# Kernel tuning notes

Measured on AMD Instinct MI355X. Metric: run time of the kernel, lower is better.

## Reference

```python
import jax, jax.numpy as jnp
import numpy as np

N_NODES = 50000
N_EDGES = 400000
LATENT = 128
HIDDEN = 512
N_HEADS = 2          # latent // 64, NodeAttn default num_heads
HEAD_DIM = LATENT // N_HEADS
N_GRAPHS = 500
LN_EPS = 1e-5


def setup_inputs() -> dict:
    key = jax.random.key(0)
    ks = jax.random.split(key, 24)
    s = 0.02
    inp = {
        "edges": jax.random.randint(ks[0], (2, N_EDGES), 0, N_NODES, dtype=jnp.int32),
        "node_feat": jax.random.normal(ks[1], (N_NODES, LATENT), jnp.float32),
        "edge_attr": jax.random.normal(ks[2], (N_EDGES, LATENT), jnp.float32),
        "u": jax.random.normal(ks[3], (N_GRAPHS, LATENT), jnp.float32),
        "num_nodes": jnp.full((N_GRAPHS,), N_NODES // N_GRAPHS, jnp.int32),
        # NodeAttn params (shared for sent/received calls, as in the module)
        "w1": jax.random.normal(ks[4], (3 * LATENT, LATENT), jnp.float32) * s,
        "b1": jnp.zeros((LATENT,), jnp.float32),
        "w2": jax.random.normal(ks[5], (N_HEADS, HEAD_DIM), jnp.float32) * s,
        "w3": jax.random.normal(ks[6], (2 * LATENT, LATENT), jnp.float32) * s,
        "b3": jnp.zeros((LATENT,), jnp.float32),
        # Encoder MLP: 4*latent -> hidden -> hidden -> latent, LN before ReLU
        "mw0": jax.random.normal(ks[7], (4 * LATENT, HIDDEN), jnp.float32) * s,
        "mb0": jnp.zeros((HIDDEN,), jnp.float32),
        "ls0": jnp.ones((HIDDEN,), jnp.float32),
        "lb0": jnp.zeros((HIDDEN,), jnp.float32),
        "mw1": jax.random.normal(ks[8], (HIDDEN, HIDDEN), jnp.float32) * s,
        "mb1": jnp.zeros((HIDDEN,), jnp.float32),
        "ls1": jnp.ones((HIDDEN,), jnp.float32),
        "lb1": jnp.zeros((HIDDEN,), jnp.float32),
        "mw2": jax.random.normal(ks[9], (HIDDEN, LATENT), jnp.float32) * s,
        "mb2": jnp.zeros((LATENT,), jnp.float32),
    }
    return inp


def _layer_norm(x, scale, bias):
    mu = jnp.mean(x, axis=-1, keepdims=True)
    var = jnp.mean(jnp.square(x - mu), axis=-1, keepdims=True)
    return (x - mu) * jax.lax.rsqrt(var + LN_EPS) * scale + bias


def _node_attn(q, k, ea, index, n_nodes, w1, b1, w2, w3, b3):
    # per-edge multi-head scores -> segment softmax over destination index -> scatter-add
    h = jax.nn.leaky_relu(jnp.concatenate([q, k, ea], axis=-1) @ w1 + b1, 0.2)
    h = h.reshape(-1, N_HEADS, HEAD_DIM)                    # [E, H, D]
    logits = jnp.einsum("ehd,hd->eh", h, w2)                 # [E, H]
    m = jax.ops.segment_max(logits, index, num_segments=n_nodes)
    m = jnp.where(jnp.isfinite(m), m, 0.0)                   # empty segments
    e = jnp.exp(logits - m[index])
    z = jax.ops.segment_sum(e, index, num_segments=n_nodes)
    alpha = e / (z[index] + 1e-16)                           # [E, H]
    v = (jnp.concatenate([k, ea], axis=-1) @ w3 + b3).reshape(-1, N_HEADS, HEAD_DIM)
    out = jax.ops.segment_sum(alpha[..., None] * v, index, num_segments=n_nodes)
    return out.reshape(n_nodes, LATENT)


def reference(edges, node_feat, edge_attr, u, num_nodes, w1, b1, w2, w3, b3,
              mw0, mb0, ls0, lb0, mw1, mb1, ls1, lb1, mw2, mb2):
    n = node_feat.shape[0]
    row, col = edges[0], edges[1]
    sent = _node_attn(node_feat[row], node_feat[col], edge_attr, row, n, w1, b1, w2, w3, b3)
    recv = _node_attn(node_feat[col], node_feat[row], edge_attr, col, n, w1, b1, w2, w3, b3)
    glob = jnp.repeat(u, num_nodes, axis=0, total_repeat_length=n)
    x = jnp.concatenate([node_feat, sent, recv, glob], axis=1)   # [N, 4*latent]
    h = jax.nn.relu(_layer_norm(x @ mw0 + mb0, ls0, lb0))
    h = jax.nn.relu(_layer_norm(h @ mw1 + mb1, ls1, lb1))
    return h @ mw2 + mb2
```

## Files before the change

### kernel.cpp

```cpp
#include <hip/hip_runtime.h>
#include <math.h>

#define LATENT 128

typedef __attribute__((ext_vector_type(8))) short bf16x8;
typedef __attribute__((ext_vector_type(4))) float f32x4;

union U4B { uint4 u; bf16x8 v; };

__device__ __forceinline__ unsigned short f2bf(float f) {
    unsigned int x = __float_as_uint(f);
    unsigned int r = (x + 0x7fffu + ((x >> 16) & 1u)) >> 16;
    return (unsigned short)r;
}
__device__ __forceinline__ float bf2f(unsigned short h) {
    return __uint_as_float(((unsigned int)h) << 16);
}

__global__ void k_gid(const int* __restrict__ num_nodes, int G, int n, int* __restrict__ gid) {
    __shared__ int goff[1025];
    if (threadIdx.x == 0) {
        int acc = 0;
        for (int g = 0; g < G; ++g) { goff[g] = acc; acc += num_nodes[g]; }
        goff[G] = acc;
    }
    __syncthreads();
    for (int g = 0; g < G; ++g) {
        int s = goff[g];
        int e = goff[g + 1]; if (e > n) e = n;
        for (int i = s + (int)threadIdx.x; i < e; i += blockDim.x) gid[i] = g;
    }
}

#define FN  1152
#define FE3 1248
#define FEV 1280
__global__ __launch_bounds__(256) void k_pack2(const float* __restrict__ mw0,
                                               const float* __restrict__ mw1,
                                               const float* __restrict__ mw2,
                                               const float* __restrict__ w1,
                                               const float* __restrict__ w3,
                                               uint4* __restrict__ pw) {
    int tid = blockIdx.x * 256 + threadIdx.x;
    if (tid >= 1312 * 64) return;
    int fid = tid >> 6, lane = tid & 63;
    const float* src; int kt, nt, N;
    if (fid < 512)       { src = mw0;            kt = fid >> 5;           nt = fid & 31;           N = 512; }
    else if (fid < 1024) { src = mw1;            kt = (fid - 512) >> 5;   nt = (fid - 512) & 31;   N = 512; }
    else if (fid < 1152) { src = mw2;            kt = (fid - 1024) >> 3;  nt = (fid - 1024) & 7;   N = 128; }
    else if (fid < 1184) { src = w1;             kt = (fid - 1152) >> 3;  nt = (fid - 1152) & 7;   N = 128; }
    else if (fid < 1216) { src = w1 + 128 * 128; kt = (fid - 1184) >> 3;  nt = (fid - 1184) & 7;   N = 128; }
    else if (fid < 1248) { src = w3;             kt = (fid - 1216) >> 3;  nt = (fid - 1216) & 7;   N = 128; }
    else if (fid < 1280) { src = w1 + 256 * 128; kt = (fid - 1248) >> 3;  nt = (fid - 1248) & 7;   N = 128; }
    else                 { src = w3 + 128 * 128; kt = (fid - 1280) >> 3;  nt = (fid - 1280) & 7;   N = 128; }
    int col = nt * 16 + (lane & 15);
    int k0 = kt * 32 + (lane >> 4) * 8;
    unsigned int w[4];
#pragma unroll
    for (int p = 0; p < 4; ++p) {
        unsigned int lo = f2bf(src[(size_t)(k0 + 2 * p) * N + col]);
        unsigned int hi = f2bf(src[(size_t)(k0 + 2 * p + 1) * N + col]);
        w[p] = lo | (hi << 16);
    }
    pw[(size_t)fid * 64 + lane] = make_uint4(w[0], w[1], w[2], w[3]);
}

__global__ void k_count(const int* __restrict__ edges, int E,
                        int* __restrict__ deg_s, int* __restrict__ deg_r) {
    int e = blockIdx.x * 256 + threadIdx.x;
    if (e < E) { atomicAdd(&deg_s[edges[e]], 1); atomicAdd(&deg_r[edges[E + e]], 1); }
}

__global__ __launch_bounds__(1024) void k_scan(const int* __restrict__ deg, int n,
                                               int* __restrict__ rowptr, int* __restrict__ cursor) {
    __shared__ int part[1025];
    int t = threadIdx.x;
    int chunk = (n + 1023) / 1024;
    int s = t * chunk, epos = s + chunk; if (epos > n) epos = n; if (s > n) s = n;
    int sum = 0;
    for (int i = s; i < epos; ++i) sum += deg[i];
    part[t] = sum;
    __syncthreads();
    if (t == 0) {
        int run = 0;
        for (int i = 0; i < 1024; ++i) { int v = part[i]; part[i] = run; run += v; }
        part[1024] = run;
    }
    __syncthreads();
    int run = part[t];
    for (int i = s; i < epos; ++i) { rowptr[i] = run; cursor[i] = run; run += deg[i]; }
    if (t == 0) rowptr[n] = part[1024];
}

__global__ void k_fill(const int* __restrict__ edges, int E,
                       int* __restrict__ cur_s, int* __restrict__ cur_r,
                       int2* __restrict__ eo_s, int2* __restrict__ eo_r) {
    int e = blockIdx.x * 256 + threadIdx.x;
    if (e < E) {
        int r = edges[e], c = edges[E + e];
        int p = atomicAdd(&cur_s[r], 1); eo_s[p] = make_int2(e, c);
        int q = atomicAdd(&cur_r[c], 1); eo_r[q] = make_int2(e, r);
    }
}

__global__ __launch_bounds__(512) void k_nodepre2(const float* __restrict__ nf, int n,
                                                  const uint4* __restrict__ pw,
                                                  unsigned short* __restrict__ PQK,
                                                  unsigned short* __restrict__ PVh) {
    __shared__ uint4 xs[32 * 64];
    int t = threadIdx.x, lane = t & 63, w = t >> 6;
    int wr = w >> 2, wc = w & 3, l15 = lane & 15, lg = lane >> 4;
    int base = blockIdx.x * 128;
#pragma unroll
    for (int it = 0; it < 4; ++it) {
        int chunk = t + it * 512;
        int row = chunk >> 4, k8 = chunk & 15, k = k8 * 8;
        int node = base + row;
        float4 v0 = make_float4(0.f, 0.f, 0.f, 0.f), v1 = v0;
        if (node < n) {
            const float4* s4 = (const float4*)(nf + (size_t)node * 128 + k);
            v0 = s4[0]; v1 = s4[1];
        }
        uint4 pk;
        pk.x = (unsigned)f2bf(v0.x) | ((unsigned)f2bf(v0.y) << 16);
        pk.y = (unsigned)f2bf(v0.z) | ((unsigned)f2bf(v0.w) << 16);
        pk.z = (unsigned)f2bf(v1.x) | ((unsigned)f2bf(v1.y) << 16);
        pk.w = (unsigned)f2bf(v1.z) | ((unsigned)f2bf(v1.w) << 16);
        int kt = k >> 5, g = (k >> 3) & 3;
        xs[(kt * 8 + (row >> 4)) * 64 + g * 16 + (row & 15)] = pk;
    }
    __syncthreads();
    f32x4 acc[4][6];
#pragma unroll
    for (int rt = 0; rt < 4; ++rt)
#pragma unroll
        for (int ct = 0; ct < 6; ++ct) acc[rt][ct] = (f32x4)(0.f);
    for (int kt = 0; kt < 4; ++kt) {
        U4B a[4];
#pragma unroll
        for (int rt = 0; rt < 4; ++rt) a[rt].u = xs[(kt * 8 + wr * 4 + rt) * 64 + lane];
        U4B b[6];
#pragma unroll
        for (int ct = 0; ct < 6; ++ct) {
            int nt = wc * 6 + ct;
            int mat = nt >> 3, ntm = nt & 7;
            b[ct].u = pw[(size_t)(FN + mat * 32 + kt * 8 + ntm) * 64 + lane];
        }
#pragma unroll
        for (int rt = 0; rt < 4; ++rt)
#pragma unroll
            for (int ct = 0; ct < 6; ++ct)
                acc[rt][ct] = __builtin_amdgcn_mfma_f32_16x16x32_bf16(a[rt].v, b[ct].v, acc[rt][ct], 0, 0, 0);
    }
#pragma unroll
    for (int rt = 0; rt < 4; ++rt)
#pragma unroll
        for (int ct = 0; ct < 6; ++ct) {
            int nt = wc * 6 + ct;
#pragma unroll
            for (int reg = 0; reg < 4; ++reg) {
                int node = base + (wr * 4 + rt) * 16 + lg * 4 + reg;
                if (node < n) {
                    unsigned short hv = f2bf(acc[rt][ct][reg]);
                    if (nt < 16) PQK[(size_t)node * 256 + nt * 16 + l15] = hv;
                    else         PVh[(size_t)node * 128 + (nt - 16) * 16 + l15] = hv;
                }
            }
        }
}

__global__ __launch_bounds__(256) void k_eproj1(const int* __restrict__ edges,
                                                const float* __restrict__ ea, int E,
                                                const uint4* __restrict__ pw,
                                                const unsigned short* __restrict__ PQK,
                                                const float* __restrict__ b1,
                                                const float* __restrict__ w2,
                                                unsigned short* __restrict__ EVg,
                                                float* __restrict__ es, float* __restrict__ er) {
    __shared__ uint4 xs[16 * 64];
    __shared__ unsigned short edata[64 * 128];
    int t = threadIdx.x, lane = t & 63, w = t >> 6;
    int wc = w, l15 = lane & 15, lg = lane >> 4;
    int base = blockIdx.x * 64;
#pragma unroll
    for (int it = 0; it < 4; ++it) {
        int chunk = t + it * 256;
        int row = chunk >> 4, k8 = chunk & 15, k = k8 * 8;
        int e = base + row;
        float4 v0 = make_float4(0.f, 0.f, 0.f, 0.f), v1 = v0;
        if (e < E) {
            const float4* s4 = (const float4*)(ea + (size_t)e * 128 + k);
            v0 = s4[0]; v1 = s4[1];
        }
        uint4 pk;
        pk.x = (unsigned)f2bf(v0.x) | ((unsigned)f2bf(v0.y) << 16);
        pk.y = (unsigned)f2bf(v0.z) | ((unsigned)f2bf(v0.w) << 16);
        pk.z = (unsigned)f2bf(v1.x) | ((unsigned)f2bf(v1.y) << 16);
        pk.w = (unsigned)f2bf(v1.z) | ((unsigned)f2bf(v1.w) << 16);
        int kt = k >> 5, g = (k >> 3) & 3;
        xs[(kt * 4 + (row >> 4)) * 64 + g * 16 + (row & 15)] = pk;
    }
    __syncthreads();
    f32x4 acc[4][4];
#pragma unroll
    for (int rt = 0; rt < 4; ++rt)
#pragma unroll
        for (int ct = 0; ct < 4; ++ct) acc[rt][ct] = (f32x4)(0.f);
    for (int kt = 0; kt < 4; ++kt) {
        U4B a[4];
#pragma unroll
        for (int rt = 0; rt < 4; ++rt) a[rt].u = xs[(kt * 4 + rt) * 64 + lane];
        U4B b[4];
        b[0].u = pw[(size_t)(FE3 + kt * 8 + wc * 2 + 0) * 64 + lane];
        b[1].u = pw[(size_t)(FE3 + kt * 8 + wc * 2 + 1) * 64 + lane];
        b[2].u = pw[(size_t)(FEV + kt * 8 + wc * 2 + 0) * 64 + lane];
        b[3].u = pw[(size_t)(FEV + kt * 8 + wc * 2 + 1) * 64 + lane];
#pragma unroll
        for (int rt = 0; rt < 4; ++rt)
#pragma unroll
            for (int ct = 0; ct < 4; ++ct)
                acc[rt][ct] = __builtin_amdgcn_mfma_f32_16x16x32_bf16(a[rt].v, b[ct].v, acc[rt][ct], 0, 0, 0);
    }
#pragma unroll
    for (int rt = 0; rt < 4; ++rt)
#pragma unroll
        for (int cc = 0; cc < 2; ++cc) {
            int col = (wc * 2 + cc) * 16 + l15;
#pragma unroll
            for (int reg = 0; reg < 4; ++reg) {
                int e_loc = rt * 16 + lg * 4 + reg;
                int e = base + e_loc;
                if (e < E) EVg[(size_t)e * 128 + col] = f2bf(acc[rt][2 + cc][reg]);
                edata[e_loc * 128 + col] = f2bf(acc[rt][cc][reg]);
            }
        }
    __syncthreads();
    int esub = lane >> 3, dg = lane & 7;
    float b1r[16], w2r[16];
    {
        const float4* b4 = (const float4*)(b1 + dg * 16);
        const float4* w4 = (const float4*)(w2 + (dg >> 2) * 64 + (dg & 3) * 16);
#pragma unroll
        for (int q = 0; q < 4; ++q) {
            float4 bv = b4[q], wv = w4[q];
            b1r[q * 4 + 0] = bv.x; b1r[q * 4 + 1] = bv.y; b1r[q * 4 + 2] = bv.z; b1r[q * 4 + 3] = bv.w;
            w2r[q * 4 + 0] = wv.x; w2r[q * 4 + 1] = wv.y; w2r[q * 4 + 2] = wv.z; w2r[q * 4 + 3] = wv.w;
        }
    }
#pragma unroll
    for (int it = 0; it < 2; ++it) {
        int e_loc = w * 16 + it * 8 + esub;
        int e = base + e_loc;
        if (e >= E) break;
        int r = edges[e], c = edges[E + e];
        const uint4* Aqr = (const uint4*)(PQK + ((size_t)r << 8) + dg * 16);
        const uint4* Akc = (const uint4*)(PQK + ((size_t)c << 8) + 128 + dg * 16);
        const uint4* Aqc = (const uint4*)(PQK + ((size_t)c << 8) + dg * 16);
        const uint4* Akr = (const uint4*)(PQK + ((size_t)r << 8) + 128 + dg * 16);
        const uint4* Ae3 = (const uint4*)(&edata[e_loc * 128 + dg * 16]);
        float ps = 0.f, pr = 0.f;
#pragma unroll
        for (int half = 0; half < 2; ++half) {
            uint4 uqr = Aqr[half], ukc = Akc[half], uqc = Aqc[half], ukr = Akr[half], ue3 = Ae3[half];
            unsigned wqr[4] = {uqr.x, uqr.y, uqr.z, uqr.w};
            unsigned wkc[4] = {ukc.x, ukc.y, ukc.z, ukc.w};
            unsigned wqc[4] = {uqc.x, uqc.y, uqc.z, uqc.w};
            unsigned wkr[4] = {ukr.x, ukr.y, ukr.z, ukr.w};
            unsigned we3[4] = {ue3.x, ue3.y, ue3.z, ue3.w};
#pragma unroll
            for (int q = 0; q < 4; ++q) {
#pragma unroll
                for (int hl = 0; hl < 2; ++hl) {
                    int i = half * 8 + q * 2 + hl;
                    float fqr = hl ? __uint_as_float(wqr[q] & 0xffff0000u) : __uint_as_float(wqr[q] << 16);
                    float fkc = hl ? __uint_as_float(wkc[q] & 0xffff0000u) : __uint_as_float(wkc[q] << 16);
                    float fqc = hl ? __uint_as_float(wqc[q] & 0xffff0000u) : __uint_as_float(wqc[q] << 16);
                    float fkr = hl ? __uint_as_float(wkr[q] & 0xffff0000u) : __uint_as_float(wkr[q] << 16);
                    float fe3 = hl ? __uint_as_float(we3[q] & 0xffff0000u) : __uint_as_float(we3[q] << 16);
                    float com = fe3 + b1r[i];
                    float hs = fqr + fkc + com; hs = hs > 0.f ? hs : 0.2f * hs;
                    float hr = fqc + fkr + com; hr = hr > 0.f ? hr : 0.2f * hr;
                    ps += hs * w2r[i]; pr += hr * w2r[i];
                }
            }
        }
        ps += __shfl_xor(ps, 1); ps += __shfl_xor(ps, 2);
        pr += __shfl_xor(pr, 1); pr += __shfl_xor(pr, 2);
        float Es = expf(ps), Er = expf(pr);
        if (dg == 0)      { es[(size_t)e * 2] = Es;     er[(size_t)e * 2] = Er; }
        else if (dg == 4) { es[(size_t)e * 2 + 1] = Es; er[(size_t)e * 2 + 1] = Er; }
    }
}

__global__ __launch_bounds__(256) void k_aggr(int E, int n,
                                              const int* __restrict__ rps, const int2* __restrict__ eo_s,
                                              const int* __restrict__ rpr, const int2* __restrict__ eo_r,
                                              const float* __restrict__ es, const float* __restrict__ er,
                                              const unsigned short* __restrict__ PVh,
                                              const unsigned short* __restrict__ EVg,
                                              const float* __restrict__ b3,
                                              float* __restrict__ out_s, float* __restrict__ out_r) {
    int w = threadIdx.x >> 6, lane = threadIdx.x & 63;
    int unit = blockIdx.x * 4 + w;
    if (unit >= 2 * n) return;
    bool sent = unit < n;
    int node = sent ? unit : unit - n;
    const int*  rp = sent ? rps : rpr;
    const int2* eo = sent ? eo_s : eo_r;
    const float* ex = sent ? es : er;
    int s0 = rp[node], s1 = rp[node + 1];
    float b3lo = b3[lane], b3hi = b3[64 + lane];
    float z0 = 0.f, z1 = 0.f, alo = 0.f, ahi = 0.f;
    int j = s0;
    for (; j + 2 <= s1; j += 2) {
        int2 pa = eo[j], pb = eo[j + 1];
        float2 ea2 = *(const float2*)&ex[(size_t)pa.x * 2];
        float2 eb2 = *(const float2*)&ex[(size_t)pb.x * 2];
        float va_lo = bf2f(PVh[(size_t)pa.y * 128 + lane])      + bf2f(EVg[(size_t)pa.x * 128 + lane])      + b3lo;
        float va_hi = bf2f(PVh[(size_t)pa.y * 128 + 64 + lane]) + bf2f(EVg[(size_t)pa.x * 128 + 64 + lane]) + b3hi;
        float vb_lo = bf2f(PVh[(size_t)pb.y * 128 + lane])      + bf2f(EVg[(size_t)pb.x * 128 + lane])      + b3lo;
        float vb_hi = bf2f(PVh[(size_t)pb.y * 128 + 64 + lane]) + bf2f(EVg[(size_t)pb.x * 128 + 64 + lane]) + b3hi;
        z0 += ea2.x + eb2.x; z1 += ea2.y + eb2.y;
        alo += ea2.x * va_lo + eb2.x * vb_lo;
        ahi += ea2.y * va_hi + eb2.y * vb_hi;
    }
    for (; j < s1; ++j) {
        int2 pa = eo[j];
        float2 ea2 = *(const float2*)&ex[(size_t)pa.x * 2];
        float va_lo = bf2f(PVh[(size_t)pa.y * 128 + lane])      + bf2f(EVg[(size_t)pa.x * 128 + lane])      + b3lo;
        float va_hi = bf2f(PVh[(size_t)pa.y * 128 + 64 + lane]) + bf2f(EVg[(size_t)pa.x * 128 + 64 + lane]) + b3hi;
        z0 += ea2.x; z1 += ea2.y;
        alo += ea2.x * va_lo; ahi += ea2.y * va_hi;
    }
    float rz0 = 1.f / (z0 + 1e-16f), rz1 = 1.f / (z1 + 1e-16f);
    float* outp = sent ? out_s : out_r;
    outp[(size_t)node * 128 + lane]      = alo * rz0;
    outp[(size_t)node * 128 + 64 + lane] = ahi * rz1;
}

__global__ __launch_bounds__(512, 4) void k_mlp3(
    const float* __restrict__ nf, const float* __restrict__ out_s, const float* __restrict__ out_r,
    const float* __restrict__ u, const int* __restrict__ gid, int n,
    const uint4* __restrict__ pw,
    const float* __restrict__ mb0, const float* __restrict__ ls0, const float* __restrict__ lb0,
    const float* __restrict__ mb1, const float* __restrict__ ls1, const float* __restrict__ lb1,
    const float* __restrict__ mb2, float* __restrict__ out) {
    extern __shared__ char smem[];
    char* hx = smem;
    float2* red = (float2*)(smem + 65536);

    int t = threadIdx.x, lane = t & 63, w = t >> 6;
    int wr = w >> 2, wc = w & 3, l15 = lane & 15, lg = lane >> 4;
    int base = blockIdx.x * 64;

#pragma unroll
    for (int it = 0; it < 16; ++it) {
        int chunk = t + it * 512;
        int row = chunk >> 7, kq = chunk & 127;
        int k = kq * 4;
        int node = base + row;
        float4 v = make_float4(0.f, 0.f, 0.f, 0.f);
        if (node < n) {
            int kk = k & 127;
            const float* src;
            if (k < 128)      src = nf    + (size_t)node * 128 + kk;
            else if (k < 256) src = out_s + (size_t)node * 128 + kk;
            else if (k < 384) src = out_r + (size_t)node * 128 + kk;
            else              src = u + (size_t)gid[node] * 128 + kk;
            v = *(const float4*)src;
        }
        uint2 p;
        p.x = (unsigned)f2bf(v.x) | ((unsigned)f2bf(v.y) << 16);
        p.y = (unsigned)f2bf(v.z) | ((unsigned)f2bf(v.w) << 16);
        int addr = (row * 1024 + k * 2) ^ ((row & 7) << 4);
        *(uint2*)(hx + addr) = p;
    }
    __syncthreads();

    f32x4 acc[2][8];
#pragma unroll
    for (int layer = 0; layer < 2; ++layer) {
        const float* MB = layer ? mb1 : mb0;
        const float* LS = layer ? ls1 : ls0;
        const float* LB = layer ? lb1 : lb0;
        const int fbase = layer ? 512 : 0;
#pragma unroll
        for (int rt = 0; rt < 2; ++rt)
#pragma unroll
            for (int ct = 0; ct < 8; ++ct) acc[rt][ct] = (f32x4)(0.f);

        for (int kt = 0; kt < 16; ++kt) {
            U4B b[8];
#pragma unroll
            for (int ct = 0; ct < 8; ++ct)
                b[ct].u = pw[(size_t)(fbase + kt * 32 + wc * 8 + ct) * 64 + lane];
            U4B a[2];
#pragma unroll
            for (int rt = 0; rt < 2; ++rt) {
                int row = wr * 32 + rt * 16 + l15;
                int addr = (row * 1024 + kt * 64 + lg * 16) ^ ((row & 7) << 4);
                a[rt].u = *(const uint4*)(hx + addr);
            }
#pragma unroll
            for (int rt = 0; rt < 2; ++rt)
#pragma unroll
                for (int ct = 0; ct < 8; ++ct)
                    acc[rt][ct] = __builtin_amdgcn_mfma_f32_16x16x32_bf16(a[rt].v, b[ct].v, acc[rt][ct], 0, 0, 0);
        }

        float mbv[8], lsv[8], lbv[8];
#pragma unroll
        for (int ct = 0; ct < 8; ++ct) {
            int col = wc * 128 + ct * 16 + l15;
            mbv[ct] = MB[col]; lsv[ct] = LS[col]; lbv[ct] = LB[col];
        }
#pragma unroll
        for (int rt = 0; rt < 2; ++rt)
#pragma unroll
            for (int reg = 0; reg < 4; ++reg) {
                float p = 0.f, q = 0.f;
#pragma unroll
                for (int ct = 0; ct < 8; ++ct) {
                    float y = acc[rt][ct][reg] + mbv[ct];
                    acc[rt][ct][reg] = y;
                    p += y; q += y * y;
                }
#pragma unroll
                for (int d = 1; d < 16; d <<= 1) { p += __shfl_xor(p, d); q += __shfl_xor(q, d); }
                if (l15 == 0) {
                    int row = wr * 32 + rt * 16 + lg * 4 + reg;
                    red[row * 4 + wc] = make_float2(p, q);
                }
            }
        __syncthreads();
#pragma unroll
        for (int rt = 0; rt < 2; ++rt)
#pragma unroll
            for (int reg = 0; reg < 4; ++reg) {
                int row = wr * 32 + rt * 16 + lg * 4 + reg;
                float2 r0 = red[row * 4 + 0], r1 = red[row * 4 + 1];
                float2 r2 = red[row * 4 + 2], r3 = red[row * 4 + 3];
                float S = r0.x + r1.x + r2.x + r3.x;
                float S2 = r0.y + r1.y + r2.y + r3.y;
                float mu = S * (1.f / 512.f);
                float var = S2 * (1.f / 512.f) - mu * mu;
                float rs = rsqrtf(var + 1e-5f);
                int rswz = (row & 7) << 4;
#pragma unroll
                for (int ct = 0; ct < 8; ++ct) {
                    float h = (acc[rt][ct][reg] - mu) * rs * lsv[ct] + lbv[ct];
                    h = fmaxf(h, 0.f);
                    int col = wc * 128 + ct * 16 + l15;
                    int addr = (row * 1024 + col * 2) ^ rswz;
                    *(unsigned short*)(hx + addr) = f2bf(h);
                }
            }
        __syncthreads();
    }

    f32x4 a2[2][2];
#pragma unroll
    for (int rt = 0; rt < 2; ++rt)
#pragma unroll
        for (int ct = 0; ct < 2; ++ct) a2[rt][ct] = (f32x4)(0.f);
    for (int kt = 0; kt < 16; ++kt) {
        U4B b[2];
#pragma unroll
        for (int ct = 0; ct < 2; ++ct)
            b[ct].u = pw[(size_t)(1024 + kt * 8 + wc * 2 + ct) * 64 + lane];
        U4B a[2];
#pragma unroll
        for (int rt = 0; rt < 2; ++rt) {
            int row = wr * 32 + rt * 16 + l15;
            int addr = (row * 1024 + kt * 64 + lg * 16) ^ ((row & 7) << 4);
            a[rt].u = *(const uint4*)(hx + addr);
        }
#pragma unroll
        for (int rt = 0; rt < 2; ++rt)
#pragma unroll
            for (int ct = 0; ct < 2; ++ct)
                a2[rt][ct] = __builtin_amdgcn_mfma_f32_16x16x32_bf16(a[rt].v, b[ct].v, a2[rt][ct], 0, 0, 0);
    }
    float mb2v[2];
#pragma unroll
    for (int ct = 0; ct < 2; ++ct) mb2v[ct] = mb2[wc * 32 + ct * 16 + l15];
#pragma unroll
    for (int rt = 0; rt < 2; ++rt)
#pragma unroll
        for (int reg = 0; reg < 4; ++reg) {
            int node = base + wr * 32 + rt * 16 + lg * 4 + reg;
            if (node < n) {
#pragma unroll
                for (int ct = 0; ct < 2; ++ct)
                    out[(size_t)node * 128 + wc * 32 + ct * 16 + l15] = a2[rt][ct][reg] + mb2v[ct];
            }
        }
}

extern "C" void kernel_launch(void* const* d_in, const int* in_sizes, int n_in,
                              void* d_out, int out_size, void* d_ws, size_t ws_size,
                              hipStream_t stream) {
    const int*   edges     = (const int*)d_in[0];
    const float* nf        = (const float*)d_in[1];
    const float* ea        = (const float*)d_in[2];
    const float* u         = (const float*)d_in[3];
    const int*   num_nodes = (const int*)d_in[4];
    const float* w1  = (const float*)d_in[5];
    const float* b1  = (const float*)d_in[6];
    const float* w2  = (const float*)d_in[7];
    const float* w3  = (const float*)d_in[8];
    const float* b3  = (const float*)d_in[9];
    const float* mw0 = (const float*)d_in[10];
    const float* mb0 = (const float*)d_in[11];
    const float* ls0 = (const float*)d_in[12];
    const float* lb0 = (const float*)d_in[13];
    const float* mw1 = (const float*)d_in[14];
    const float* mb1 = (const float*)d_in[15];
    const float* ls1 = (const float*)d_in[16];
    const float* lb1 = (const float*)d_in[17];
    const float* mw2 = (const float*)d_in[18];
    const float* mb2 = (const float*)d_in[19];

    int E = in_sizes[0] / 2;
    int n = in_sizes[1] / LATENT;
    int G = in_sizes[4];
    float* out = (float*)d_out;

    char* wsb = (char*)d_ws;
    size_t off = 0;
    auto alloc = [&](size_t bytes) { void* p = (void*)(wsb + off); off += (bytes + 15) & ~(size_t)15; return p; };
    uint4*          pw    = (uint4*)alloc((size_t)1312 * 64 * 16);
    unsigned short* PQK   = (unsigned short*)alloc((size_t)n * 256 * 2);
    unsigned short* PVh   = (unsigned short*)alloc((size_t)n * 128 * 2);
    unsigned short* EVg   = (unsigned short*)alloc((size_t)E * 128 * 2);
    float*          es    = (float*)alloc((size_t)E * 2 * 4);
    float*          er    = (float*)alloc((size_t)E * 2 * 4);
    float*          out_s = (float*)alloc((size_t)n * 128 * 4);
    float*          out_r = (float*)alloc((size_t)n * 128 * 4);
    int*            gid   = (int*)alloc((size_t)n * 4);
    int*            deg_s = (int*)alloc((size_t)n * 4);
    int*            deg_r = (int*)alloc((size_t)n * 4);
    int*            cur_s = (int*)alloc((size_t)n * 4);
    int*            cur_r = (int*)alloc((size_t)n * 4);
    int*            rps   = (int*)alloc((size_t)(n + 1) * 4);
    int*            rpr   = (int*)alloc((size_t)(n + 1) * 4);
    int2*           eo_s  = (int2*)alloc((size_t)E * 8);
    int2*           eo_r  = (int2*)alloc((size_t)E * 8);

    hipMemsetAsync(deg_s, 0, (size_t)2 * n * 4 + 16, stream);

    hipFuncSetAttribute((const void*)k_mlp3, hipFuncAttributeMaxDynamicSharedMemorySize, 67584);

    k_gid<<<1, 256, 0, stream>>>(num_nodes, G, n, gid);
    k_pack2<<<(1312 * 64 + 255) / 256, 256, 0, stream>>>(mw0, mw1, mw2, w1, w3, pw);
    k_count<<<(E + 255) / 256, 256, 0, stream>>>(edges, E, deg_s, deg_r);
    k_scan<<<1, 1024, 0, stream>>>(deg_s, n, rps, cur_s);
    k_scan<<<1, 1024, 0, stream>>>(deg_r, n, rpr, cur_r);
    k_fill<<<(E + 255) / 256, 256, 0, stream>>>(edges, E, cur_s, cur_r, eo_s, eo_r);
    k_nodepre2<<<(n + 127) / 128, 512, 0, stream>>>(nf, n, pw, PQK, PVh);
    k_eproj1<<<(E + 63) / 64, 256, 0, stream>>>(edges, ea, E, pw, PQK, b1, w2, EVg, es, er);
    k_aggr<<<(2 * n + 3) / 4, 256, 0, stream>>>(E, n, rps, eo_s, rpr, eo_r,
                                                es, er, PVh, EVg, b3, out_s, out_r);
    k_mlp3<<<(n + 63) / 64, 512, 67584, stream>>>(nf, out_s, out_r, u, gid, n, pw,
                                                  mb0, ls0, lb0, mb1, ls1, lb1, mb2, out);
}
```

Before: 902.2 us.

## Store scores in CSR order, bf16 aggregate outputs, nontemporal loads/stores, 4-way unrolled aggregation

k_fill now records each edge's CSR slot, so k_eproj1 writes exp scores directly in sorted order and k_aggr reads them contiguously instead of gathering them by edge id. k_aggr loads packed bf16 pairs per lane, unrolls four edges at a time, and writes its outputs as bf16, which halves the intermediate traffic into k_mlp3. Streaming loads and stores across several kernels use nontemporal hints. The cost is two extra E-sized index arrays and scattered 4-byte score writes in k_eproj1, plus bf16 rounding of the aggregated messages.

Result: no change. 901.1 us (-0.1%).

```diff
diff --git a/kernel.cpp b/kernel.cpp
--- a/kernel.cpp
+++ b/kernel.cpp
@@ -5,8 +5,14 @@
 
 typedef __attribute__((ext_vector_type(8))) short bf16x8;
 typedef __attribute__((ext_vector_type(4))) float f32x4;
+typedef __attribute__((ext_vector_type(2))) float f32x2;
+typedef __attribute__((ext_vector_type(2))) int i32x2;
+typedef __attribute__((ext_vector_type(2))) unsigned u32x2;
 
 union U4B { uint4 u; bf16x8 v; };
+
+template <typename T>
+__device__ __forceinline__ T ntl(const T* p) { return __builtin_nontemporal_load(p); }
 
 __device__ __forceinline__ unsigned short f2bf(float f) {
     unsigned int x = __float_as_uint(f);
@@ -15,6 +21,9 @@
 }
 __device__ __forceinline__ float bf2f(unsigned short h) {
     return __uint_as_float(((unsigned int)h) << 16);
+}
+__device__ __forceinline__ unsigned pk2(float a, float b) {
+    return (unsigned)f2bf(a) | ((unsigned)f2bf(b) << 16);
 }
 
 __global__ void k_gid(const int* __restrict__ num_nodes, int G, int n, int* __restrict__ gid) {
@@ -94,12 +103,13 @@
 
 __global__ void k_fill(const int* __restrict__ edges, int E,
                        int* __restrict__ cur_s, int* __restrict__ cur_r,
-                       int2* __restrict__ eo_s, int2* __restrict__ eo_r) {
+                       int2* __restrict__ eo_s, int2* __restrict__ eo_r,
+                       int* __restrict__ sm_s, int* __restrict__ sm_r) {
     int e = blockIdx.x * 256 + threadIdx.x;
     if (e < E) {
         int r = edges[e], c = edges[E + e];
-        int p = atomicAdd(&cur_s[r], 1); eo_s[p] = make_int2(e, c);
-        int q = atomicAdd(&cur_r[c], 1); eo_r[q] = make_int2(e, r);
+        int p = atomicAdd(&cur_s[r], 1); eo_s[p] = make_int2(e, c); sm_s[e] = p;
+        int q = atomicAdd(&cur_r[c], 1); eo_r[q] = make_int2(e, r); sm_r[e] = q;
     }
 }
 
@@ -116,18 +126,16 @@
         int chunk = t + it * 512;
         int row = chunk >> 4, k8 = chunk & 15, k = k8 * 8;
         int node = base + row;
-        float4 v0 = make_float4(0.f, 0.f, 0.f, 0.f), v1 = v0;
+        f32x4 v0 = (f32x4)(0.f), v1 = (f32x4)(0.f);
         if (node < n) {
-            const float4* s4 = (const float4*)(nf + (size_t)node * 128 + k);
-            v0 = s4[0]; v1 = s4[1];
-        }
-        uint4 pk;
-        pk.x = (unsigned)f2bf(v0.x) | ((unsigned)f2bf(v0.y) << 16);
-        pk.y = (unsigned)f2bf(v0.z) | ((unsigned)f2bf(v0.w) << 16);
-        pk.z = (unsigned)f2bf(v1.x) | ((unsigned)f2bf(v1.y) << 16);
-        pk.w = (unsigned)f2bf(v1.z) | ((unsigned)f2bf(v1.w) << 16);
+            const f32x4* s4 = (const f32x4*)(nf + (size_t)node * 128 + k);
+            v0 = ntl(s4); v1 = ntl(s4 + 1);
+        }
+        uint4 pkv;
+        pkv.x = pk2(v0.x, v0.y); pkv.y = pk2(v0.z, v0.w);
+        pkv.z = pk2(v1.x, v1.y); pkv.w = pk2(v1.z, v1.w);
         int kt = k >> 5, g = (k >> 3) & 3;
-        xs[(kt * 8 + (row >> 4)) * 64 + g * 16 + (row & 15)] = pk;
+        xs[(kt * 8 + (row >> 4)) * 64 + g * 16 + (row & 15)] = pkv;
     }
     __syncthreads();
     f32x4 acc[4][6];
@@ -175,8 +183,10 @@
                                                 const unsigned short* __restrict__ PQK,
                                                 const float* __restrict__ b1,
                                                 const float* __restrict__ w2,
+                                                const int* __restrict__ sm_s,
+                                                const int* __restrict__ sm_r,
                                                 unsigned short* __restrict__ EVg,
-                                                float* __restrict__ es, float* __restrict__ er) {
+                                                float* __restrict__ ess2, float* __restrict__ ers2) {
     __shared__ uint4 xs[16 * 64];
     __shared__ unsigned short edata[64 * 128];
     int t = threadIdx.x, lane = t & 63, w = t >> 6;
@@ -187,18 +197,16 @@
         int chunk = t + it * 256;
         int row = chunk >> 4, k8 = chunk & 15, k = k8 * 8;
         int e = base + row;
-        float4 v0 = make_float4(0.f, 0.f, 0.f, 0.f), v1 = v0;
+        f32x4 v0 = (f32x4)(0.f), v1 = (f32x4)(0.f);
         if (e < E) {
-            const float4* s4 = (const float4*)(ea + (size_t)e * 128 + k);
-            v0 = s4[0]; v1 = s4[1];
-        }
-        uint4 pk;
-        pk.x = (unsigned)f2bf(v0.x) | ((unsigned)f2bf(v0.y) << 16);
-        pk.y = (unsigned)f2bf(v0.z) | ((unsigned)f2bf(v0.w) << 16);
-        pk.z = (unsigned)f2bf(v1.x) | ((unsigned)f2bf(v1.y) << 16);
-        pk.w = (unsigned)f2bf(v1.z) | ((unsigned)f2bf(v1.w) << 16);
+            const f32x4* s4 = (const f32x4*)(ea + (size_t)e * 128 + k);
+            v0 = ntl(s4); v1 = ntl(s4 + 1);
+        }
+        uint4 pkv;
+        pkv.x = pk2(v0.x, v0.y); pkv.y = pk2(v0.z, v0.w);
+        pkv.z = pk2(v1.x, v1.y); pkv.w = pk2(v1.z, v1.w);
         int kt = k >> 5, g = (k >> 3) & 3;
-        xs[(kt * 4 + (row >> 4)) * 64 + g * 16 + (row & 15)] = pk;
+        xs[(kt * 4 + (row >> 4)) * 64 + g * 16 + (row & 15)] = pkv;
     }
     __syncthreads();
     f32x4 acc[4][4];
@@ -230,7 +238,8 @@
             for (int reg = 0; reg < 4; ++reg) {
                 int e_loc = rt * 16 + lg * 4 + reg;
                 int e = base + e_loc;
-                if (e < E) EVg[(size_t)e * 128 + col] = f2bf(acc[rt][2 + cc][reg]);
+                if (e < E) __builtin_nontemporal_store(f2bf(acc[rt][2 + cc][reg]),
+                                                       &EVg[(size_t)e * 128 + col]);
                 edata[e_loc * 128 + col] = f2bf(acc[rt][cc][reg]);
             }
         }
@@ -287,59 +296,79 @@
         ps += __shfl_xor(ps, 1); ps += __shfl_xor(ps, 2);
         pr += __shfl_xor(pr, 1); pr += __shfl_xor(pr, 2);
         float Es = expf(ps), Er = expf(pr);
-        if (dg == 0)      { es[(size_t)e * 2] = Es;     er[(size_t)e * 2] = Er; }
-        else if (dg == 4) { es[(size_t)e * 2 + 1] = Es; er[(size_t)e * 2 + 1] = Er; }
+        if (dg == 0) {
+            __builtin_nontemporal_store(Es, &ess2[(size_t)sm_s[e] * 2]);
+            __builtin_nontemporal_store(Er, &ers2[(size_t)sm_r[e] * 2]);
+        } else if (dg == 4) {
+            __builtin_nontemporal_store(Es, &ess2[(size_t)sm_s[e] * 2 + 1]);
+            __builtin_nontemporal_store(Er, &ers2[(size_t)sm_r[e] * 2 + 1]);
+        }
     }
 }
 
 __global__ __launch_bounds__(256) void k_aggr(int E, int n,
                                               const int* __restrict__ rps, const int2* __restrict__ eo_s,
                                               const int* __restrict__ rpr, const int2* __restrict__ eo_r,
-                                              const float* __restrict__ es, const float* __restrict__ er,
+                                              const float* __restrict__ ess2, const float* __restrict__ ers2,
                                               const unsigned short* __restrict__ PVh,
                                               const unsigned short* __restrict__ EVg,
                                               const float* __restrict__ b3,
-                                              float* __restrict__ out_s, float* __restrict__ out_r) {
+                                              unsigned short* __restrict__ out_sh,
+                                              unsigned short* __restrict__ out_rh) {
     int w = threadIdx.x >> 6, lane = threadIdx.x & 63;
     int unit = blockIdx.x * 4 + w;
     if (unit >= 2 * n) return;
     bool sent = unit < n;
     int node = sent ? unit : unit - n;
-    const int*  rp = sent ? rps : rpr;
-    const int2* eo = sent ? eo_s : eo_r;
-    const float* ex = sent ? es : er;
+    const int*   rp = sent ? rps : rpr;
+    const i32x2* eo = (const i32x2*)(sent ? eo_s : eo_r);
+    const float* ex = sent ? ess2 : ers2;
     int s0 = rp[node], s1 = rp[node + 1];
-    float b3lo = b3[lane], b3hi = b3[64 + lane];
-    float z0 = 0.f, z1 = 0.f, alo = 0.f, ahi = 0.f;
+    float b3a = b3[2 * lane], b3b = b3[2 * lane + 1];
+    const unsigned* EV32 = (const unsigned*)EVg;
+    const unsigned* PV32 = (const unsigned*)PVh;
+    float z0 = 0.f, z1 = 0.f, acca = 0.f, accb = 0.f;
     int j = s0;
-    for (; j + 2 <= s1; j += 2) {
-        int2 pa = eo[j], pb = eo[j + 1];
-        float2 ea2 = *(const float2*)&ex[(size_t)pa.x * 2];
-        float2 eb2 = *(const float2*)&ex[(size_t)pb.x * 2];
-        float va_lo = bf2f(PVh[(size_t)pa.y * 128 + lane])      + bf2f(EVg[(size_t)pa.x * 128 + lane])      + b3lo;
-        float va_hi = bf2f(PVh[(size_t)pa.y * 128 + 64 + lane]) + bf2f(EVg[(size_t)pa.x * 128 + 64 + lane]) + b3hi;
-        float vb_lo = bf2f(PVh[(size_t)pb.y * 128 + lane])      + bf2f(EVg[(size_t)pb.x * 128 + lane])      + b3lo;
-        float vb_hi = bf2f(PVh[(size_t)pb.y * 128 + 64 + lane]) + bf2f(EVg[(size_t)pb.x * 128 + 64 + lane]) + b3hi;
-        z0 += ea2.x + eb2.x; z1 += ea2.y + eb2.y;
-        alo += ea2.x * va_lo + eb2.x * vb_lo;
-        ahi += ea2.y * va_hi + eb2.y * vb_hi;
+    for (; j + 4 <= s1; j += 4) {
+        i32x2 p[4]; f32x2 ez[4]; unsigned ev[4], pv[4];
+#pragma unroll
+        for (int q = 0; q < 4; ++q) p[q] = ntl(eo + j + q);
+#pragma unroll
+        for (int q = 0; q < 4; ++q) ez[q] = ntl((const f32x2*)(ex + 2 * (j + q)));
+#pragma unroll
+        for (int q = 0; q < 4; ++q) ev[q] = ntl(EV32 + (size_t)p[q].x * 64 + lane);
+#pragma unroll
+        for (int q = 0; q < 4; ++q) pv[q] = PV32[(size_t)p[q].y * 64 + lane];
+#pragma unroll
+        for (int q = 0; q < 4; ++q) {
+            float va = __uint_as_float(ev[q] << 16) + __uint_as_float(pv[q] << 16) + b3a;
+            float vb = __uint_as_float(ev[q] & 0xffff0000u) + __uint_as_float(pv[q] & 0xffff0000u) + b3b;
+            z0 += ez[q].x; z1 += ez[q].y;
+            float aw = (lane < 32) ? ez[q].x : ez[q].y;
+            acca += aw * va; accb += aw * vb;
+        }
     }
     for (; j < s1; ++j) {
-        int2 pa = eo[j];
-        float2 ea2 = *(const float2*)&ex[(size_t)pa.x * 2];
-        float va_lo = bf2f(PVh[(size_t)pa.y * 128 + lane])      + bf2f(EVg[(size_t)pa.x * 128 + lane])      + b3lo;
-        float va_hi = bf2f(PVh[(size_t)pa.y * 128 + 64 + lane]) + bf2f(EVg[(size_t)pa.x * 128 + 64 + lane]) + b3hi;
-        z0 += ea2.x; z1 += ea2.y;
-        alo += ea2.x * va_lo; ahi += ea2.y * va_hi;
-    }
-    float rz0 = 1.f / (z0 + 1e-16f), rz1 = 1.f / (z1 + 1e-16f);
-    float* outp = sent ? out_s : out_r;
-    outp[(size_t)node * 128 + lane]      = alo * rz0;
-    outp[(size_t)node * 128 + 64 + lane] = ahi * rz1;
+        i32x2 p = ntl(eo + j);
+        f32x2 ez = ntl((const f32x2*)(ex + 2 * j));
+        unsigned ev = ntl(EV32 + (size_t)p.x * 64 + lane);
+        unsigned pv = PV32[(size_t)p.y * 64 + lane];
+        float va = __uint_as_float(ev << 16) + __uint_as_float(pv << 16) + b3a;
+        float vb = __uint_as_float(ev & 0xffff0000u) + __uint_as_float(pv & 0xffff0000u) + b3b;
+        z0 += ez.x; z1 += ez.y;
+        float aw = (lane < 32) ? ez.x : ez.y;
+        acca += aw * va; accb += aw * vb;
+    }
+    float zz = (lane < 32) ? z0 : z1;
+    float rz = 1.f / (zz + 1e-16f);
+    unsigned o = pk2(acca * rz, accb * rz);
+    unsigned* outp = (unsigned*)(sent ? out_sh : out_rh);
+    outp[(size_t)node * 64 + lane] = o;
 }
 
 __global__ __launch_bounds__(512, 4) void k_mlp3(
-    const float* __restrict__ nf, const float* __restrict__ out_s, const float* __restrict__ out_r,
+    const float* __restrict__ nf, const unsigned short* __restrict__ out_sh,
+    const unsigned short* __restrict__ out_rh,
     const float* __restrict__ u, const int* __restrict__ gid, int n,
     const uint4* __restrict__ pw,
     const float* __restrict__ mb0, const float* __restrict__ ls0, const float* __restrict__ lb0,
@@ -359,21 +388,22 @@
         int row = chunk >> 7, kq = chunk & 127;
         int k = kq * 4;
         int node = base + row;
-        float4 v = make_float4(0.f, 0.f, 0.f, 0.f);
+        u32x2 p = (u32x2)(0u);
         if (node < n) {
             int kk = k & 127;
-            const float* src;
-            if (k < 128)      src = nf    + (size_t)node * 128 + kk;
-            else if (k < 256) src = out_s + (size_t)node * 128 + kk;
-            else if (k < 384) src = out_r + (size_t)node * 128 + kk;
-            else              src = u + (size_t)gid[node] * 128 + kk;
-            v = *(const float4*)src;
-        }
-        uint2 p;
-        p.x = (unsigned)f2bf(v.x) | ((unsigned)f2bf(v.y) << 16);
-        p.y = (unsigned)f2bf(v.z) | ((unsigned)f2bf(v.w) << 16);
+            if (k < 128) {
+                f32x4 v = ntl((const f32x4*)(nf + (size_t)node * 128 + kk));
+                p.x = pk2(v.x, v.y); p.y = pk2(v.z, v.w);
+            } else if (k < 384) {
+                const unsigned short* s = (k < 256 ? out_sh : out_rh) + (size_t)node * 128 + kk;
+                p = ntl((const u32x2*)s);
+            } else {
+                f32x4 v = *(const f32x4*)(u + (size_t)gid[node] * 128 + kk);
+                p.x = pk2(v.x, v.y); p.y = pk2(v.z, v.w);
+            }
+        }
         int addr = (row * 1024 + k * 2) ^ ((row & 7) << 4);
-        *(uint2*)(hx + addr) = p;
+        *(u32x2*)(hx + addr) = p;
     }
     __syncthreads();
 
@@ -492,7 +522,8 @@
             if (node < n) {
 #pragma unroll
                 for (int ct = 0; ct < 2; ++ct)
-                    out[(size_t)node * 128 + wc * 32 + ct * 16 + l15] = a2[rt][ct][reg] + mb2v[ct];
+                    __builtin_nontemporal_store(a2[rt][ct][reg] + mb2v[ct],
+                        &out[(size_t)node * 128 + wc * 32 + ct * 16 + l15]);
             }
         }
 }
@@ -529,23 +560,25 @@
     char* wsb = (char*)d_ws;
     size_t off = 0;
     auto alloc = [&](size_t bytes) { void* p = (void*)(wsb + off); off += (bytes + 15) & ~(size_t)15; return p; };
-    uint4*          pw    = (uint4*)alloc((size_t)1312 * 64 * 16);
-    unsigned short* PQK   = (unsigned short*)alloc((size_t)n * 256 * 2);
-    unsigned short* PVh   = (unsigned short*)alloc((size_t)n * 128 * 2);
-    unsigned short* EVg   = (unsigned short*)alloc((size_t)E * 128 * 2);
-    float*          es    = (float*)alloc((size_t)E * 2 * 4);
-    float*          er    = (float*)alloc((size_t)E * 2 * 4);
-    float*          out_s = (float*)alloc((size_t)n * 128 * 4);
-    float*          out_r = (float*)alloc((size_t)n * 128 * 4);
-    int*            gid   = (int*)alloc((size_t)n * 4);
-    int*            deg_s = (int*)alloc((size_t)n * 4);
-    int*            deg_r = (int*)alloc((size_t)n * 4);
-    int*            cur_s = (int*)alloc((size_t)n * 4);
-    int*            cur_r = (int*)alloc((size_t)n * 4);
-    int*            rps   = (int*)alloc((size_t)(n + 1) * 4);
-    int*            rpr   = (int*)alloc((size_t)(n + 1) * 4);
-    int2*           eo_s  = (int2*)alloc((size_t)E * 8);
-    int2*           eo_r  = (int2*)alloc((size_t)E * 8);
+    uint4*          pw     = (uint4*)alloc((size_t)1312 * 64 * 16);
+    unsigned short* PQK    = (unsigned short*)alloc((size_t)n * 256 * 2);
+    unsigned short* PVh    = (unsigned short*)alloc((size_t)n * 128 * 2);
+    unsigned short* EVg    = (unsigned short*)alloc((size_t)E * 128 * 2);
+    float*          ess2   = (float*)alloc((size_t)E * 2 * 4);
+    float*          ers2   = (float*)alloc((size_t)E * 2 * 4);
+    unsigned short* out_sh = (unsigned short*)alloc((size_t)n * 128 * 2);
+    unsigned short* out_rh = (unsigned short*)alloc((size_t)n * 128 * 2);
+    int*            gid    = (int*)alloc((size_t)n * 4);
+    int*            deg_s  = (int*)alloc((size_t)n * 4);
+    int*            deg_r  = (int*)alloc((size_t)n * 4);
+    int*            cur_s  = (int*)alloc((size_t)n * 4);
+    int*            cur_r  = (int*)alloc((size_t)n * 4);
+    int*            rps    = (int*)alloc((size_t)(n + 1) * 4);
+    int*            rpr    = (int*)alloc((size_t)(n + 1) * 4);
+    int2*           eo_s   = (int2*)alloc((size_t)E * 8);
+    int2*           eo_r   = (int2*)alloc((size_t)E * 8);
+    int*            sm_s   = (int*)alloc((size_t)E * 4);
+    int*            sm_r   = (int*)alloc((size_t)E * 4);
 
     hipMemsetAsync(deg_s, 0, (size_t)2 * n * 4 + 16, stream);
 
@@ -556,11 +589,12 @@
     k_count<<<(E + 255) / 256, 256, 0, stream>>>(edges, E, deg_s, deg_r);
     k_scan<<<1, 1024, 0, stream>>>(deg_s, n, rps, cur_s);
     k_scan<<<1, 1024, 0, stream>>>(deg_r, n, rpr, cur_r);
-    k_fill<<<(E + 255) / 256, 256, 0, stream>>>(edges, E, cur_s, cur_r, eo_s, eo_r);
+    k_fill<<<(E + 255) / 256, 256, 0, stream>>>(edges, E, cur_s, cur_r, eo_s, eo_r, sm_s, sm_r);
     k_nodepre2<<<(n + 127) / 128, 512, 0, stream>>>(nf, n, pw, PQK, PVh);
-    k_eproj1<<<(E + 63) / 64, 256, 0, stream>>>(edges, ea, E, pw, PQK, b1, w2, EVg, es, er);
+    k_eproj1<<<(E + 63) / 64, 256, 0, stream>>>(edges, ea, E, pw, PQK, b1, w2, sm_s, sm_r,
+                                                EVg, ess2, ers2);
     k_aggr<<<(2 * n + 3) / 4, 256, 0, stream>>>(E, n, rps, eo_s, rpr, eo_r,
-                                                es, er, PVh, EVg, b3, out_s, out_r);
-    k_mlp3<<<(n + 63) / 64, 512, 67584, stream>>>(nf, out_s, out_r, u, gid, n, pw,
+                                                ess2, ers2, PVh, EVg, b3, out_sh, out_rh);
+    k_mlp3<<<(n + 63) / 64, 512, 67584, stream>>>(nf, out_sh, out_rh, u, gid, n, pw,
                                                   mb0, ls0, lb0, mb1, ls1, lb1, mb2, out);
 }
```
